# Performance work log

Hardware: AMD Instinct MI355X
Metric: run time of the kernel (lower is better)

Reference implementation:

```python
import jax, jax.numpy as jnp
import numpy as np

B, SX, SY, H = 4, 512, 512, 128


def setup_inputs() -> dict:
    key = jax.random.key(0)
    k1, k2, k3, k4, k5 = jax.random.split(key, 5)
    x = jax.random.normal(k1, (B, SX, 2 * H), dtype=jnp.float32)
    y = jax.random.normal(k2, (B, SY, 2 * H), dtype=jnp.float32)
    # nn.Linear(in, out, bias=False) weight has shape (out, in)
    s = 1.0 / np.sqrt(2 * H)
    Wc1 = jax.random.uniform(k3, (H, 2 * H), minval=-s, maxval=s, dtype=jnp.float32)
    Wc2 = jax.random.uniform(k4, (H, 2 * H), minval=-s, maxval=s, dtype=jnp.float32)
    sv = 1.0 / np.sqrt(H)
    vc = jax.random.uniform(k5, (1, H), minval=-sv, maxval=sv, dtype=jnp.float32)
    return {"x": x, "y": y, "Wc1": Wc1, "Wc2": Wc2, "vc": vc}


def reference(x, y, Wc1, Wc2, vc):
    # s1: (B, Sx, H), s2: (B, Sy, H)
    s1 = jnp.einsum('bsd,hd->bsh', x, Wc1)
    s2 = jnp.einsum('btd,hd->bth', y, Wc2)
    # broadcast tanh-MLP score: (B, Sy, Sx, H) -> (B, Sy, Sx)
    sjt = jnp.einsum('btsh,h->bts', jnp.tanh(s1[:, None, :, :] + s2[:, :, None, :]), vc[0])
    ait = jax.nn.softmax(sjt, axis=2)  # softmax over Sx
    qtc = jnp.einsum('bts,bsd->btd', ait, x)  # (B, Sy, 2H)
    return qtc
```

## Files before the change

kernel.cpp:

```cpp
#include <hip/hip_runtime.h>


#define NB 4
#define SEQ 512
#define HDIM 128
#define DDIM 256

static constexpr float TWO_LOG2E = 2.8853900817779268f;
static constexpr float LOG2E     = 1.4426950408889634f;

__device__ __forceinline__ void gload_lds16(const void* g, void* l) {
    __builtin_amdgcn_global_load_lds(
        (const __attribute__((address_space(1))) void*)g,
        (__attribute__((address_space(3))) void*)l, 16, 0, 0);
}

__global__ __launch_bounds__(256) void proj_part_kernel(
    const float* __restrict__ x, const float* __restrict__ y,
    const float* __restrict__ W1, const float* __restrict__ W2,
    float* __restrict__ part)
{
    __shared__ float As[1024];
    __shared__ float sPr[8192];
    const int tid = threadIdx.x;
    const int blk = blockIdx.x;
    const int kq  = blk >> 9;
    const int gr0 = (blk & 511) * 8;

    const float* in; const float* W; int srow;
    if (gr0 < 2048) { in = x; W = W1; srow = gr0; }
    else            { in = y; W = W2; srow = gr0 - 2048; }

    {
        const int r = tid >> 5, kk = tid & 31;
        *(float4*)&As[tid * 4] =
            *(const float4*)&in[(srow + r) * 256 + kq * 128 + kk * 4];
    }
    __syncthreads();

    const int hq = tid & 31;
    const int ks = tid >> 5;

    float4 acc4[8];
    #pragma unroll
    for (int r = 0; r < 8; ++r) acc4[r] = make_float4(0.f, 0.f, 0.f, 0.f);

    #pragma unroll
    for (int u = 0; u < 4; ++u) {
        const int kof = kq * 128 + ks * 16 + u * 4;
        const float4 w0 = *(const float4*)&W[(4*hq + 0) * 256 + kof];
        const float4 w1 = *(const float4*)&W[(4*hq + 1) * 256 + kof];
        const float4 w2 = *(const float4*)&W[(4*hq + 2) * 256 + kof];
        const float4 w3 = *(const float4*)&W[(4*hq + 3) * 256 + kof];
        #pragma unroll
        for (int r = 0; r < 8; ++r) {
            const float4 a = *(const float4*)&As[r * 128 + ks * 16 + u * 4];
            acc4[r].x = fmaf(a.w,w0.w, fmaf(a.z,w0.z, fmaf(a.y,w0.y, fmaf(a.x,w0.x, acc4[r].x))));
            acc4[r].y = fmaf(a.w,w1.w, fmaf(a.z,w1.z, fmaf(a.y,w1.y, fmaf(a.x,w1.x, acc4[r].y))));
            acc4[r].z = fmaf(a.w,w2.w, fmaf(a.z,w2.z, fmaf(a.y,w2.y, fmaf(a.x,w2.x, acc4[r].z))));
            acc4[r].w = fmaf(a.w,w3.w, fmaf(a.z,w3.z, fmaf(a.y,w3.y, fmaf(a.x,w3.x, acc4[r].w))));
        }
    }
    #pragma unroll
    for (int r = 0; r < 8; ++r)
        *(float4*)&sPr[ks * 1024 + r * 128 + hq * 4] = acc4[r];
    __syncthreads();
    {
        const int r = tid >> 5, h4 = (tid & 31) * 4;
        float4 s = make_float4(0.f, 0.f, 0.f, 0.f);
        #pragma unroll
        for (int k2 = 0; k2 < 8; ++k2) {
            const float4 p = *(const float4*)&sPr[k2 * 1024 + r * 128 + h4];
            s.x += p.x; s.y += p.y; s.z += p.z; s.w += p.w;
        }
        *(float4*)&part[kq * 524288 + (gr0 + r) * 128 + h4] = s;
    }
}

__global__ __launch_bounds__(256) void proj_combine_kernel(
    const float* __restrict__ part,
    float* __restrict__ e1sw, float* __restrict__ e2)
{
    const int j = blockIdx.x * 256 + threadIdx.x;
    const float4 p0 = ((const float4*)part)[j];
    const float4 p1 = ((const float4*)part)[j + 131072];
    float4 o;
    o.x = __builtin_amdgcn_exp2f((p0.x + p1.x) * TWO_LOG2E);
    o.y = __builtin_amdgcn_exp2f((p0.y + p1.y) * TWO_LOG2E);
    o.z = __builtin_amdgcn_exp2f((p0.z + p1.z) * TWO_LOG2E);
    o.w = __builtin_amdgcn_exp2f((p0.w + p1.w) * TWO_LOG2E);
    const int gr = j >> 5;
    const int hq = j & 31;
    if (gr < 2048) {
        const int b = gr >> 9, s = gr & 511;
        const int c = s >> 6, sl = s & 63;
        ((float4*)e1sw)[((b * 8 + c) * 32 + hq) * 64 + (sl ^ hq)] = o;
    } else {
        ((float4*)e2)[j - 65536] = o;
    }
}

__global__ __launch_bounds__(1024) void score_kernel(
    const float* __restrict__ e1sw, const float* __restrict__ e2g,
    const float* __restrict__ vc,  float* __restrict__ P)
{
    __shared__ float4 sE1[2][2048];
    __shared__ float  sScore[4 * 512];
    __shared__ float  sPartC[2][1024];

    const int tid  = threadIdx.x;
    const int b    = blockIdx.x >> 7;
    const int t0   = (blockIdx.x & 127) * 4;
    const int w    = tid >> 6;
    const int lane = tid & 63;
    const int wu   = __builtin_amdgcn_readfirstlane(w);
    const int tU   = wu >> 2;
    const int qU   = wu & 3;

    float4 vcs[8];
    float4 e2s[8];
    #pragma unroll
    for (int j = 0; j < 8; ++j) {
        vcs[j] = *(const float4*)&vc[(qU * 8 + j) * 4];
        e2s[j] = *(const float4*)&e2g[(b * SEQ + t0 + tU) * HDIM + (qU * 8 + j) * 4];
    }

    const float4* e1c = (const float4*)e1sw + b * 16384;

    #pragma unroll
    for (int j = 0; j < 2; ++j) {
        const int seg = wu * 128 + j * 64;
        gload_lds16(e1c + seg + lane, &sE1[0][seg]);
    }

    for (int c = 0; c < 8; ++c) {
        __syncthreads();
        if (c < 7) {
            const float4* gch = e1c + (c + 1) * 2048;
            #pragma unroll
            for (int j = 0; j < 2; ++j) {
                const int seg = wu * 128 + j * 64;
                gload_lds16(gch + seg + lane, &sE1[(c + 1) & 1][seg]);
            }
        }
        if (c > 0 && tid < 256) {
            const int t = tid >> 6, s = tid & 63;
            const float* pc = sPartC[(c - 1) & 1];
            const float r = pc[(t*4+0)*64 + s] + pc[(t*4+1)*64 + s]
                          + pc[(t*4+2)*64 + s] + pc[(t*4+3)*64 + s];
            sScore[t * 512 + (c - 1) * 64 + s] = -2.f * r;
        }
        float acc = 0.f;
        const float4* buf = sE1[c & 1];
        #pragma unroll
        for (int j = 0; j < 8; ++j) {
            const int hq = qU * 8 + j;
            const float4 e1 = buf[hq * 64 + (lane ^ hq)];
            const float4 vv = vcs[j];
            const float4 e2 = e2s[j];
            const float f1 = fmaf(e1.x, e2.x, 1.f);
            const float f2 = fmaf(e1.y, e2.y, 1.f);
            const float f3 = fmaf(e1.z, e2.z, 1.f);
            const float f4 = fmaf(e1.w, e2.w, 1.f);
            const float f12 = f1 * f2, f34 = f3 * f4;
            const float n12 = fmaf(vv.x, f2, vv.y * f1);
            const float n34 = fmaf(vv.z, f4, vv.w * f3);
            const float num = fmaf(n12, f34, n34 * f12);
            acc = fmaf(num, __builtin_amdgcn_rcpf(f12 * f34), acc);
        }
        sPartC[c & 1][w * 64 + lane] = acc;
    }
    __syncthreads();
    if (tid < 256) {
        const int t = tid >> 6, s = tid & 63;
        const float* pc = sPartC[7 & 1];
        const float r = pc[(t*4+0)*64 + s] + pc[(t*4+1)*64 + s]
                      + pc[(t*4+2)*64 + s] + pc[(t*4+3)*64 + s];
        sScore[t * 512 + 7 * 64 + s] = -2.f * r;
    }
    __syncthreads();

    if (w < 4) {
        float v[8];
        float m = -1e30f;
        #pragma unroll
        for (int j = 0; j < 8; ++j) {
            v[j] = sScore[w * 512 + lane + j * 64];
            m = fmaxf(m, v[j]);
        }
        #pragma unroll
        for (int off = 32; off; off >>= 1) m = fmaxf(m, __shfl_xor(m, off));
        float sum = 0.f;
        #pragma unroll
        for (int j = 0; j < 8; ++j) {
            v[j] = __builtin_amdgcn_exp2f((v[j] - m) * LOG2E);
            sum += v[j];
        }
        #pragma unroll
        for (int off = 32; off; off >>= 1) sum += __shfl_xor(sum, off);
        const float inv = __builtin_amdgcn_rcpf(sum);
        float* Prow = &P[(b * SEQ + t0 + w) * SEQ];
        #pragma unroll
        for (int j = 0; j < 8; ++j)
            Prow[lane + j * 64] = v[j] * inv;
    }
}

__global__ __launch_bounds__(256) void pax_kernel(
    const float* __restrict__ P, const float* __restrict__ x,
    float* __restrict__ out)
{
    __shared__ float sP[SEQ * 8];
    __shared__ float sRed[4 * 8 * DDIM];
    const int tid = threadIdx.x;
    const int b   = blockIdx.x >> 6;
    const int t0  = (blockIdx.x & 63) * 8;
    const int w    = tid >> 6;
    const int lane = tid & 63;

    #pragma unroll
    for (int j = 0; j < 4; ++j) {
        const int i = tid + j * 256;
        const int t = i >> 7, c4 = i & 127;
        const float4 p = *(const float4*)&P[(b * SEQ + t0 + t) * SEQ + c4 * 4];
        sP[(c4 * 4 + 0) * 8 + t] = p.x;
        sP[(c4 * 4 + 1) * 8 + t] = p.y;
        sP[(c4 * 4 + 2) * 8 + t] = p.z;
        sP[(c4 * 4 + 3) * 8 + t] = p.w;
    }
    __syncthreads();

    const float4* x4 = (const float4*)x;
    float4 acc[8];
    #pragma unroll
    for (int t = 0; t < 8; ++t) acc[t] = make_float4(0.f, 0.f, 0.f, 0.f);

    #pragma unroll 4
    for (int si = 0; si < 128; ++si) {
        const int s = w * 128 + si;
        const float4 xv  = x4[(b * SEQ + s) * 64 + lane];
        const float4 p03 = *(const float4*)&sP[s * 8];
        const float4 p47 = *(const float4*)&sP[s * 8 + 4];
        acc[0].x = fmaf(p03.x, xv.x, acc[0].x); acc[0].y = fmaf(p03.x, xv.y, acc[0].y);
        acc[0].z = fmaf(p03.x, xv.z, acc[0].z); acc[0].w = fmaf(p03.x, xv.w, acc[0].w);
        acc[1].x = fmaf(p03.y, xv.x, acc[1].x); acc[1].y = fmaf(p03.y, xv.y, acc[1].y);
        acc[1].z = fmaf(p03.y, xv.z, acc[1].z); acc[1].w = fmaf(p03.y, xv.w, acc[1].w);
        acc[2].x = fmaf(p03.z, xv.x, acc[2].x); acc[2].y = fmaf(p03.z, xv.y, acc[2].y);
        acc[2].z = fmaf(p03.z, xv.z, acc[2].z); acc[2].w = fmaf(p03.z, xv.w, acc[2].w);
        acc[3].x = fmaf(p03.w, xv.x, acc[3].x); acc[3].y = fmaf(p03.w, xv.y, acc[3].y);
        acc[3].z = fmaf(p03.w, xv.z, acc[3].z); acc[3].w = fmaf(p03.w, xv.w, acc[3].w);
        acc[4].x = fmaf(p47.x, xv.x, acc[4].x); acc[4].y = fmaf(p47.x, xv.y, acc[4].y);
        acc[4].z = fmaf(p47.x, xv.z, acc[4].z); acc[4].w = fmaf(p47.x, xv.w, acc[4].w);
        acc[5].x = fmaf(p47.y, xv.x, acc[5].x); acc[5].y = fmaf(p47.y, xv.y, acc[5].y);
        acc[5].z = fmaf(p47.y, xv.z, acc[5].z); acc[5].w = fmaf(p47.y, xv.w, acc[5].w);
        acc[6].x = fmaf(p47.z, xv.x, acc[6].x); acc[6].y = fmaf(p47.z, xv.y, acc[6].y);
        acc[6].z = fmaf(p47.z, xv.z, acc[6].z); acc[6].w = fmaf(p47.z, xv.w, acc[6].w);
        acc[7].x = fmaf(p47.w, xv.x, acc[7].x); acc[7].y = fmaf(p47.w, xv.y, acc[7].y);
        acc[7].z = fmaf(p47.w, xv.z, acc[7].z); acc[7].w = fmaf(p47.w, xv.w, acc[7].w);
    }
    __syncthreads();
    float4* sRed4 = (float4*)sRed;
    #pragma unroll
    for (int t = 0; t < 8; ++t)
        sRed4[w * 512 + t * 64 + lane] = acc[t];
    __syncthreads();
    #pragma unroll
    for (int j = 0; j < 8; ++j) {
        const int i = tid + j * 256;
        const int t = i >> 8, d = i & 255;
        const float r = sRed[0*2048 + t*256 + d] + sRed[1*2048 + t*256 + d]
                      + sRed[2*2048 + t*256 + d] + sRed[3*2048 + t*256 + d];
        out[(b * SEQ + t0 + t) * DDIM + d] = r;
    }
}

extern "C" void kernel_launch(void* const* d_in, const int* in_sizes, int n_in,
                              void* d_out, int out_size, void* d_ws, size_t ws_size,
                              hipStream_t stream) {
    const float* x   = (const float*)d_in[0];
    const float* y   = (const float*)d_in[1];
    const float* W1  = (const float*)d_in[2];
    const float* W2  = (const float*)d_in[3];
    const float* vc  = (const float*)d_in[4];
    float* outp = (float*)d_out;

    float* ws   = (float*)d_ws;
    float* e1   = ws;
    float* e2   = ws + NB * SEQ * HDIM;
    float* part = ws + 2 * NB * SEQ * HDIM;
    float* P    = ws + 2 * NB * SEQ * HDIM + 2 * 4096 * HDIM;

    hipLaunchKernelGGL(proj_part_kernel,    dim3(1024), dim3(256), 0, stream,
                       x, y, W1, W2, part);
    hipLaunchKernelGGL(proj_combine_kernel, dim3(512),  dim3(256), 0, stream,
                       part, e1, e2);
    hipLaunchKernelGGL(score_kernel,        dim3(512),  dim3(1024), 0, stream,
                       e1, e2, vc, P);
    hipLaunchKernelGGL(pax_kernel,          dim3(256),  dim3(256), 0, stream,
                       P, x, outp);
}
```

Baseline: 115.4 us.

## Fuse projection kernels, reassign score work by head group, widen pax blocks

Merges the split-K projection and the combine step into one kernel that covers the full K=256 per block and applies the exp transform directly, removing the partial-sum buffer round trip and one launch. The score kernel now gives each wave two head quads across all four query rows and reduces through LDS atomicAdd instead of a staged partial-sum buffer. The pax kernel doubles its threads to 512, halving each wave's sequence chunk and widening the reduction. Trade-offs are fewer projection blocks (512), LDS atomic contention in the score kernel, and larger LDS use in pax.

```diff
diff --git a/kernel.cpp b/kernel.cpp
--- a/kernel.cpp
+++ b/kernel.cpp
@@ -15,26 +15,26 @@
         (__attribute__((address_space(3))) void*)l, 16, 0, 0);
 }
 
-__global__ __launch_bounds__(256) void proj_part_kernel(
+__global__ __launch_bounds__(256) void proj_kernel(
     const float* __restrict__ x, const float* __restrict__ y,
     const float* __restrict__ W1, const float* __restrict__ W2,
-    float* __restrict__ part)
+    float* __restrict__ e1sw, float* __restrict__ e2)
 {
-    __shared__ float As[1024];
+    __shared__ float As[2048];
     __shared__ float sPr[8192];
     const int tid = threadIdx.x;
-    const int blk = blockIdx.x;
-    const int kq  = blk >> 9;
-    const int gr0 = (blk & 511) * 8;
+    const int gr0 = blockIdx.x * 8;
 
     const float* in; const float* W; int srow;
     if (gr0 < 2048) { in = x; W = W1; srow = gr0; }
     else            { in = y; W = W2; srow = gr0 - 2048; }
 
-    {
-        const int r = tid >> 5, kk = tid & 31;
-        *(float4*)&As[tid * 4] =
-            *(const float4*)&in[(srow + r) * 256 + kq * 128 + kk * 4];
+    #pragma unroll
+    for (int j = 0; j < 2; ++j) {
+        const int idx = tid + j * 256;
+        const int r = idx >> 6, kk = idx & 63;
+        *(float4*)&As[idx * 4] =
+            *(const float4*)&in[(srow + r) * 256 + kk * 4];
     }
     __syncthreads();
 
@@ -46,15 +46,15 @@
     for (int r = 0; r < 8; ++r) acc4[r] = make_float4(0.f, 0.f, 0.f, 0.f);
 
     #pragma unroll
-    for (int u = 0; u < 4; ++u) {
-        const int kof = kq * 128 + ks * 16 + u * 4;
+    for (int u = 0; u < 8; ++u) {
+        const int kof = ks * 32 + u * 4;
         const float4 w0 = *(const float4*)&W[(4*hq + 0) * 256 + kof];
         const float4 w1 = *(const float4*)&W[(4*hq + 1) * 256 + kof];
         const float4 w2 = *(const float4*)&W[(4*hq + 2) * 256 + kof];
         const float4 w3 = *(const float4*)&W[(4*hq + 3) * 256 + kof];
         #pragma unroll
         for (int r = 0; r < 8; ++r) {
-            const float4 a = *(const float4*)&As[r * 128 + ks * 16 + u * 4];
+            const float4 a = *(const float4*)&As[r * 256 + kof];
             acc4[r].x = fmaf(a.w,w0.w, fmaf(a.z,w0.z, fmaf(a.y,w0.y, fmaf(a.x,w0.x, acc4[r].x))));
             acc4[r].y = fmaf(a.w,w1.w, fmaf(a.z,w1.z, fmaf(a.y,w1.y, fmaf(a.x,w1.x, acc4[r].y))));
             acc4[r].z = fmaf(a.w,w2.w, fmaf(a.z,w2.z, fmaf(a.y,w2.y, fmaf(a.x,w2.x, acc4[r].z))));
@@ -66,37 +66,26 @@
         *(float4*)&sPr[ks * 1024 + r * 128 + hq * 4] = acc4[r];
     __syncthreads();
     {
-        const int r = tid >> 5, h4 = (tid & 31) * 4;
+        const int r = tid >> 5, h4 = tid & 31;
         float4 s = make_float4(0.f, 0.f, 0.f, 0.f);
         #pragma unroll
         for (int k2 = 0; k2 < 8; ++k2) {
-            const float4 p = *(const float4*)&sPr[k2 * 1024 + r * 128 + h4];
+            const float4 p = *(const float4*)&sPr[k2 * 1024 + r * 128 + h4 * 4];
             s.x += p.x; s.y += p.y; s.z += p.z; s.w += p.w;
         }
-        *(float4*)&part[kq * 524288 + (gr0 + r) * 128 + h4] = s;
-    }
-}
-
-__global__ __launch_bounds__(256) void proj_combine_kernel(
-    const float* __restrict__ part,
-    float* __restrict__ e1sw, float* __restrict__ e2)
-{
-    const int j = blockIdx.x * 256 + threadIdx.x;
-    const float4 p0 = ((const float4*)part)[j];
-    const float4 p1 = ((const float4*)part)[j + 131072];
-    float4 o;
-    o.x = __builtin_amdgcn_exp2f((p0.x + p1.x) * TWO_LOG2E);
-    o.y = __builtin_amdgcn_exp2f((p0.y + p1.y) * TWO_LOG2E);
-    o.z = __builtin_amdgcn_exp2f((p0.z + p1.z) * TWO_LOG2E);
-    o.w = __builtin_amdgcn_exp2f((p0.w + p1.w) * TWO_LOG2E);
-    const int gr = j >> 5;
-    const int hq = j & 31;
-    if (gr < 2048) {
-        const int b = gr >> 9, s = gr & 511;
-        const int c = s >> 6, sl = s & 63;
-        ((float4*)e1sw)[((b * 8 + c) * 32 + hq) * 64 + (sl ^ hq)] = o;
-    } else {
-        ((float4*)e2)[j - 65536] = o;
+        float4 o;
+        o.x = __builtin_amdgcn_exp2f(s.x * TWO_LOG2E);
+        o.y = __builtin_amdgcn_exp2f(s.y * TWO_LOG2E);
+        o.z = __builtin_amdgcn_exp2f(s.z * TWO_LOG2E);
+        o.w = __builtin_amdgcn_exp2f(s.w * TWO_LOG2E);
+        const int gr = gr0 + r;
+        if (gr < 2048) {
+            const int b = gr >> 9, ss = gr & 511;
+            const int c = ss >> 6, sl = ss & 63;
+            ((float4*)e1sw)[((b * 8 + c) * 32 + h4) * 64 + (sl ^ h4)] = o;
+        } else {
+            ((float4*)e2)[(gr - 2048) * 32 + h4] = o;
+        }
     }
 }
 
@@ -106,7 +95,6 @@
 {
     __shared__ float4 sE1[2][2048];
     __shared__ float  sScore[4 * 512];
-    __shared__ float  sPartC[2][1024];
 
     const int tid  = threadIdx.x;
     const int b    = blockIdx.x >> 7;
@@ -114,16 +102,21 @@
     const int w    = tid >> 6;
     const int lane = tid & 63;
     const int wu   = __builtin_amdgcn_readfirstlane(w);
-    const int tU   = wu >> 2;
-    const int qU   = wu & 3;
-
-    float4 vcs[8];
-    float4 e2s[8];
-    #pragma unroll
-    for (int j = 0; j < 8; ++j) {
-        vcs[j] = *(const float4*)&vc[(qU * 8 + j) * 4];
-        e2s[j] = *(const float4*)&e2g[(b * SEQ + t0 + tU) * HDIM + (qU * 8 + j) * 4];
-    }
+    const int hg   = wu;
+
+    float4 vcs[2];
+    float4 e2s[4][2];
+    #pragma unroll
+    for (int j = 0; j < 2; ++j)
+        vcs[j] = *(const float4*)&vc[(hg * 2 + j) * 4];
+    #pragma unroll
+    for (int t = 0; t < 4; ++t)
+        #pragma unroll
+        for (int j = 0; j < 2; ++j)
+            e2s[t][j] = *(const float4*)&e2g[(b * SEQ + t0 + t) * HDIM + (hg * 2 + j) * 4];
+
+    sScore[tid] = 0.f;
+    sScore[tid + 1024] = 0.f;
 
     const float4* e1c = (const float4*)e1sw + b * 16384;
 
@@ -143,40 +136,36 @@
                 gload_lds16(gch + seg + lane, &sE1[(c + 1) & 1][seg]);
             }
         }
-        if (c > 0 && tid < 256) {
-            const int t = tid >> 6, s = tid & 63;
-            const float* pc = sPartC[(c - 1) & 1];
-            const float r = pc[(t*4+0)*64 + s] + pc[(t*4+1)*64 + s]
-                          + pc[(t*4+2)*64 + s] + pc[(t*4+3)*64 + s];
-            sScore[t * 512 + (c - 1) * 64 + s] = -2.f * r;
-        }
-        float acc = 0.f;
+        float acc0 = 0.f, acc1 = 0.f, acc2 = 0.f, acc3 = 0.f;
         const float4* buf = sE1[c & 1];
         #pragma unroll
-        for (int j = 0; j < 8; ++j) {
-            const int hq = qU * 8 + j;
+        for (int j = 0; j < 2; ++j) {
+            const int hq = hg * 2 + j;
             const float4 e1 = buf[hq * 64 + (lane ^ hq)];
             const float4 vv = vcs[j];
-            const float4 e2 = e2s[j];
-            const float f1 = fmaf(e1.x, e2.x, 1.f);
-            const float f2 = fmaf(e1.y, e2.y, 1.f);
-            const float f3 = fmaf(e1.z, e2.z, 1.f);
-            const float f4 = fmaf(e1.w, e2.w, 1.f);
-            const float f12 = f1 * f2, f34 = f3 * f4;
-            const float n12 = fmaf(vv.x, f2, vv.y * f1);
-            const float n34 = fmaf(vv.z, f4, vv.w * f3);
-            const float num = fmaf(n12, f34, n34 * f12);
-            acc = fmaf(num, __builtin_amdgcn_rcpf(f12 * f34), acc);
-        }
-        sPartC[c & 1][w * 64 + lane] = acc;
-    }
-    __syncthreads();
-    if (tid < 256) {
-        const int t = tid >> 6, s = tid & 63;
-        const float* pc = sPartC[7 & 1];
-        const float r = pc[(t*4+0)*64 + s] + pc[(t*4+1)*64 + s]
-                      + pc[(t*4+2)*64 + s] + pc[(t*4+3)*64 + s];
-        sScore[t * 512 + 7 * 64 + s] = -2.f * r;
+            #pragma unroll
+            for (int t = 0; t < 4; ++t) {
+                const float4 e2 = e2s[t][j];
+                const float f1 = fmaf(e1.x, e2.x, 1.f);
+                const float f2 = fmaf(e1.y, e2.y, 1.f);
+                const float f3 = fmaf(e1.z, e2.z, 1.f);
+                const float f4 = fmaf(e1.w, e2.w, 1.f);
+                const float f12 = f1 * f2, f34 = f3 * f4;
+                const float n12 = fmaf(vv.x, f2, vv.y * f1);
+                const float n34 = fmaf(vv.z, f4, vv.w * f3);
+                const float num = fmaf(n12, f34, n34 * f12);
+                const float r = fmaf(num, __builtin_amdgcn_rcpf(f12 * f34),
+                                     (t == 0) ? acc0 : (t == 1) ? acc1 : (t == 2) ? acc2 : acc3);
+                if      (t == 0) acc0 = r;
+                else if (t == 1) acc1 = r;
+                else if (t == 2) acc2 = r;
+                else             acc3 = r;
+            }
+        }
+        atomicAdd(&sScore[0 * 512 + c * 64 + lane], acc0);
+        atomicAdd(&sScore[1 * 512 + c * 64 + lane], acc1);
+        atomicAdd(&sScore[2 * 512 + c * 64 + lane], acc2);
+        atomicAdd(&sScore[3 * 512 + c * 64 + lane], acc3);
     }
     __syncthreads();
 
@@ -185,7 +174,7 @@
         float m = -1e30f;
         #pragma unroll
         for (int j = 0; j < 8; ++j) {
-            v[j] = sScore[w * 512 + lane + j * 64];
+            v[j] = -2.f * sScore[w * 512 + lane + j * 64];
             m = fmaxf(m, v[j]);
         }
         #pragma unroll
@@ -206,12 +195,12 @@
     }
 }
 
-__global__ __launch_bounds__(256) void pax_kernel(
+__global__ __launch_bounds__(512) void pax_kernel(
     const float* __restrict__ P, const float* __restrict__ x,
     float* __restrict__ out)
 {
     __shared__ float sP[SEQ * 8];
-    __shared__ float sRed[4 * 8 * DDIM];
+    __shared__ float sRed[8 * 8 * DDIM];
     const int tid = threadIdx.x;
     const int b   = blockIdx.x >> 6;
     const int t0  = (blockIdx.x & 63) * 8;
@@ -219,8 +208,8 @@
     const int lane = tid & 63;
 
     #pragma unroll
-    for (int j = 0; j < 4; ++j) {
-        const int i = tid + j * 256;
+    for (int j = 0; j < 2; ++j) {
+        const int i = tid + j * 512;
         const int t = i >> 7, c4 = i & 127;
         const float4 p = *(const float4*)&P[(b * SEQ + t0 + t) * SEQ + c4 * 4];
         sP[(c4 * 4 + 0) * 8 + t] = p.x;
@@ -236,8 +225,8 @@
     for (int t = 0; t < 8; ++t) acc[t] = make_float4(0.f, 0.f, 0.f, 0.f);
 
     #pragma unroll 4
-    for (int si = 0; si < 128; ++si) {
-        const int s = w * 128 + si;
+    for (int si = 0; si < 64; ++si) {
+        const int s = w * 64 + si;
         const float4 xv  = x4[(b * SEQ + s) * 64 + lane];
         const float4 p03 = *(const float4*)&sP[s * 8];
         const float4 p47 = *(const float4*)&sP[s * 8 + 4];
@@ -265,11 +254,13 @@
         sRed4[w * 512 + t * 64 + lane] = acc[t];
     __syncthreads();
     #pragma unroll
-    for (int j = 0; j < 8; ++j) {
-        const int i = tid + j * 256;
+    for (int j = 0; j < 4; ++j) {
+        const int i = tid + j * 512;
         const int t = i >> 8, d = i & 255;
         const float r = sRed[0*2048 + t*256 + d] + sRed[1*2048 + t*256 + d]
-                      + sRed[2*2048 + t*256 + d] + sRed[3*2048 + t*256 + d];
+                      + sRed[2*2048 + t*256 + d] + sRed[3*2048 + t*256 + d]
+                      + sRed[4*2048 + t*256 + d] + sRed[5*2048 + t*256 + d]
+                      + sRed[6*2048 + t*256 + d] + sRed[7*2048 + t*256 + d];
         out[(b * SEQ + t0 + t) * DDIM + d] = r;
     }
 }
@@ -284,18 +275,15 @@
     const float* vc  = (const float*)d_in[4];
     float* outp = (float*)d_out;
 
-    float* ws   = (float*)d_ws;
-    float* e1   = ws;
-    float* e2   = ws + NB * SEQ * HDIM;
-    float* part = ws + 2 * NB * SEQ * HDIM;
-    float* P    = ws + 2 * NB * SEQ * HDIM + 2 * 4096 * HDIM;
-
-    hipLaunchKernelGGL(proj_part_kernel,    dim3(1024), dim3(256), 0, stream,
-                       x, y, W1, W2, part);
-    hipLaunchKernelGGL(proj_combine_kernel, dim3(512),  dim3(256), 0, stream,
-                       part, e1, e2);
-    hipLaunchKernelGGL(score_kernel,        dim3(512),  dim3(1024), 0, stream,
+    float* ws = (float*)d_ws;
+    float* e1 = ws;
+    float* e2 = ws + NB * SEQ * HDIM;
+    float* P  = ws + 2 * NB * SEQ * HDIM;
+
+    hipLaunchKernelGGL(proj_kernel,  dim3(512), dim3(256),  0, stream,
+                       x, y, W1, W2, e1, e2);
+    hipLaunchKernelGGL(score_kernel, dim3(512), dim3(1024), 0, stream,
                        e1, e2, vc, P);
-    hipLaunchKernelGGL(pax_kernel,          dim3(256),  dim3(256), 0, stream,
+    hipLaunchKernelGGL(pax_kernel,   dim3(256), dim3(512),  0, stream,
                        P, x, outp);
 }
```

New measurement: 183.6 us. 1.59x slower.
